# Kernel optimization log

Measured on AMD Instinct MI355X. Metric: run time of the kernel, lower is better.

The kernel has to match this reference:

```python
import jax, jax.numpy as jnp
import numpy as np

B, S, R, H = 64, 256, 196, 1024

def setup_inputs() -> dict:
    key = jax.random.key(0)
    ks = jax.random.split(key, 12)
    s = 0.02
    return {
        "dns_feature": jax.random.normal(ks[0], (B, S, H), jnp.float32),
        "img_features": jax.random.normal(ks[1], (B, R, H), jnp.float32),
        "W_dns1": jax.random.normal(ks[2], (H, H), jnp.float32) * s,
        "b_dns1": jax.random.normal(ks[3], (H,), jnp.float32) * s,
        "W_img1": jax.random.normal(ks[4], (H, H), jnp.float32) * s,
        "w_att1": jax.random.normal(ks[5], (2 * H,), jnp.float32) * s,
        "b_att1": jax.random.normal(ks[6], (), jnp.float32) * s,
        "W_dns2": jax.random.normal(ks[7], (H, H), jnp.float32) * s,
        "W_img2": jax.random.normal(ks[8], (H, H), jnp.float32) * s,
        "b_img2": jax.random.normal(ks[9], (H,), jnp.float32) * s,
        "w_att2": jax.random.normal(ks[10], (2 * H,), jnp.float32) * s,
        "b_att2": jax.random.normal(ks[11], (), jnp.float32) * s,
    }

def reference(dns_feature, img_features, W_dns1, b_dns1, W_img1, w_att1, b_att1,
              W_dns2, W_img2, b_img2, w_att2, b_att2):
    h = W_dns1.shape[0]
    # --- stage 1: textual attention (img queries over dns positions) ---
    # tanh(concat([img_proj, dns_proj])) then 2H->1 linear decomposes into
    # per-side dot products + broadcast add (repeat is position-wise redundant).
    dns_p1 = jnp.tanh(jnp.einsum('bsh,oh->bso', dns_feature, W_dns1) + b_dns1)  # (B,S,H)
    img_p1 = jnp.tanh(jnp.einsum('brh,oh->bro', img_features, W_img1))          # (B,R,H)
    s_img = img_p1 @ w_att1[:h]   # (B,R)  concat order: [img, dns]
    s_dns = dns_p1 @ w_att1[h:]   # (B,S)
    scores1 = s_img[:, :, None] + s_dns[:, None, :] + b_att1                    # (B,R,S)
    a1 = jax.nn.softmax(scores1, axis=-1)
    att_dns = jnp.einsum('brs,bsh->brh', a1, dns_feature)                       # (B,R,H)
    # --- stage 2: visual attention (attended-dns queries over img regions) ---
    dns_p2 = jnp.tanh(jnp.einsum('brh,oh->bro', att_dns, W_dns2))               # (B,R,H)
    img_p2 = jnp.tanh(jnp.einsum('brh,oh->bro', img_features, W_img2) + b_img2) # (B,R,H)
    t_dns = dns_p2 @ w_att2[:h]   # (B,R)  concat order: [dns, img]
    t_img = img_p2 @ w_att2[h:]   # (B,R)
    scores2 = t_dns[:, :, None] + t_img[:, None, :] + b_att2                    # (B,R,R)
    a2 = jax.nn.softmax(scores2, axis=-1)
    att_img = jnp.einsum('bij,bjh->bih', a2, img_features)                      # (B,R,H)
    return att_img, att_dns
```

## Files before the change

### kernel.cpp

```cpp
#include <hip/hip_runtime.h>

#define Hdim 1024
#define BB 64
#define SS 256
#define RR 196
#define MD (BB * SS)
#define MI (BB * RR)

typedef __attribute__((ext_vector_type(8))) short short8;
typedef __attribute__((ext_vector_type(4))) float floatx4;
typedef unsigned short us;

__device__ __forceinline__ unsigned short f2bf(float f) {
  unsigned int u = __float_as_uint(f);
  unsigned int r = 0x7FFFu + ((u >> 16) & 1u);
  return (unsigned short)((u + r) >> 16);
}

__device__ __forceinline__ float fast_tanh(float x) {
  x = fminf(15.f, fmaxf(-15.f, x));
  float e = __expf(2.f * x);
  return (e - 1.f) / (e + 1.f);
}

#define GLOAD16(g, l) __builtin_amdgcn_global_load_lds( \
    (const __attribute__((address_space(1))) unsigned int*)(g), \
    (__attribute__((address_space(3))) unsigned int*)(l), 16, 0, 0)

__global__ __launch_bounds__(256) void prep_kernel(
    const float4* __restrict__ dns, const float4* __restrict__ img,
    const float4* __restrict__ Wd1, const float4* __restrict__ Wi2,
    uint4* __restrict__ dns_bf, uint4* __restrict__ img_bf,
    uint4* __restrict__ wd1_bf, uint4* __restrict__ wi2_bf,
    float4* __restrict__ scz)
{
  constexpr int N0 = (MD * Hdim) / 8;
  constexpr int N1 = N0 + (MI * Hdim) / 8;
  constexpr int N2 = N1 + (Hdim * Hdim) / 8;
  constexpr int N3 = N2 + (Hdim * Hdim) / 8;
  constexpr int N4 = N3 + (MD + MI) / 8;
  const int stride = gridDim.x * 256;
  for (int i = blockIdx.x * 256 + threadIdx.x; i < N4; i += stride) {
    if (i < N3) {
      const float4* src; uint4* dst; int li;
      if (i < N0)      { src = dns; dst = dns_bf; li = i; }
      else if (i < N1) { src = img; dst = img_bf; li = i - N0; }
      else if (i < N2) { src = Wd1; dst = wd1_bf; li = i - N1; }
      else             { src = Wi2; dst = wi2_bf; li = i - N2; }
      const float4 a = src[2 * li];
      const float4 b = src[2 * li + 1];
      uint4 o;
      o.x = (unsigned)f2bf(a.x) | ((unsigned)f2bf(a.y) << 16);
      o.y = (unsigned)f2bf(a.z) | ((unsigned)f2bf(a.w) << 16);
      o.z = (unsigned)f2bf(b.x) | ((unsigned)f2bf(b.y) << 16);
      o.w = (unsigned)f2bf(b.z) | ((unsigned)f2bf(b.w) << 16);
      dst[li] = o;
    } else {
      const int li = i - N3;
      const float4 z4 = {0.f, 0.f, 0.f, 0.f};
      scz[2 * li]     = z4;
      scz[2 * li + 1] = z4;
    }
  }
}

__global__ __launch_bounds__(256) void gemm_score_bf2(
    const us* __restrict__ X1, const us* __restrict__ W1,
    const float* __restrict__ bias1, const float* __restrict__ v1, float* sc1,
    const us* __restrict__ X2, const us* __restrict__ W2,
    const float* __restrict__ bias2, const float* __restrict__ v2, float* sc2)
{
  __shared__ us Ash[2][128 * 64];
  __shared__ us Bsh[2][128 * 64];

  const int q  = gridDim.x >> 3;
  const int wg = (blockIdx.x & 7) * q + (blockIdx.x >> 3);

  const us* Xb; const us* Wb; const float* bias; const float* vatt; float* scores;
  int mt, nt;
  if (wg < (MD / 128) * 8) {
    Xb = X1; Wb = W1; bias = bias1; vatt = v1; scores = sc1;
    mt = wg >> 3; nt = wg & 7;
  } else {
    const int w2 = wg - (MD / 128) * 8;
    Xb = X2; Wb = W2; bias = bias2; vatt = v2; scores = sc2;
    mt = w2 >> 3; nt = w2 & 7;
  }
  const long m0 = (long)mt * 128;
  const long n0 = (long)nt * 128;

  const int tid  = threadIdx.x;
  const int lane = tid & 63;
  const int wave = tid >> 6;
  const int waveM = (wave >> 1) * 64;
  const int waveN = (wave & 1) * 64;

  const int rowSub  = lane >> 3;
  const int srcColE = (((lane & 7) ^ rowSub)) * 8;

  const us* gA[4]; const us* gB[4];
  int ldst[4];
  #pragma unroll
  for (int c = 0; c < 4; ++c) {
    const int r = (wave * 4 + c) * 8 + rowSub;
    gA[c] = Xb + (m0 + r) * Hdim + srcColE;
    gB[c] = Wb + (n0 + r) * Hdim + srcColE;
    ldst[c] = (wave * 4 + c) * 512 + lane * 8;
  }

  floatx4 acc[4][4];
  #pragma unroll
  for (int i = 0; i < 4; ++i)
    #pragma unroll
    for (int j = 0; j < 4; ++j)
      acc[i][j] = (floatx4){0.f, 0.f, 0.f, 0.f};

  const int frow = lane & 15;
  const int g    = lane >> 4;
  const int sw   = frow & 7;

  #pragma unroll
  for (int c = 0; c < 4; ++c) {
    GLOAD16(gA[c], &Ash[0][ldst[c]]);
    GLOAD16(gB[c], &Bsh[0][ldst[c]]);
  }
  __syncthreads();

  auto kstep = [&](int t, int pb) {
    if (t < 15) {
      const int k0 = (t + 1) * 64;
      #pragma unroll
      for (int c = 0; c < 4; ++c) {
        GLOAD16(gA[c] + k0, &Ash[pb ^ 1][ldst[c]]);
        GLOAD16(gB[c] + k0, &Bsh[pb ^ 1][ldst[c]]);
      }
    }
    #pragma unroll
    for (int ks = 0; ks < 2; ++ks) {
      const int slot = ((ks * 4 + g) ^ sw) * 8;
      short8 afr[4], bfr[4];
      #pragma unroll
      for (int mf = 0; mf < 4; ++mf)
        afr[mf] = *(const short8*)(&Ash[pb][0] + (waveM + mf * 16 + frow) * 64 + slot);
      #pragma unroll
      for (int nf = 0; nf < 4; ++nf)
        bfr[nf] = *(const short8*)(&Bsh[pb][0] + (waveN + nf * 16 + frow) * 64 + slot);
      #pragma unroll
      for (int mf = 0; mf < 4; ++mf)
        #pragma unroll
        for (int nf = 0; nf < 4; ++nf)
          acc[mf][nf] = __builtin_amdgcn_mfma_f32_16x16x32_bf16(afr[mf], bfr[nf], acc[mf][nf], 0, 0, 0);
    }
    __syncthreads();
  };

  for (int t2 = 0; t2 < 8; ++t2) {
    kstep(t2 * 2, 0);
    kstep(t2 * 2 + 1, 1);
  }

  const int rgrp = lane >> 4;
  #pragma unroll
  for (int mf = 0; mf < 4; ++mf) {
    float part[4] = {0.f, 0.f, 0.f, 0.f};
    #pragma unroll
    for (int nf = 0; nf < 4; ++nf) {
      const int n = (int)n0 + waveN + nf * 16 + (lane & 15);
      const float bi = bias[n];
      const float vv = vatt[n];
      #pragma unroll
      for (int j = 0; j < 4; ++j)
        part[j] += fast_tanh(acc[mf][nf][j] + bi) * vv;
    }
    #pragma unroll
    for (int j = 0; j < 4; ++j) {
      float s = part[j];
      s += __shfl_xor(s, 1);
      s += __shfl_xor(s, 2);
      s += __shfl_xor(s, 4);
      s += __shfl_xor(s, 8);
      if ((lane & 15) == 0) {
        const int m = (int)m0 + waveM + mf * 16 + rgrp * 4 + j;
        atomicAdd(&scores[m], s);
      }
    }
  }
}

__global__ __launch_bounds__(256) void attend_bcast(
    const float* __restrict__ sc_d, const us* __restrict__ dns_bf,
    const float* __restrict__ sc_i, const us* __restrict__ img_bf,
    float* __restrict__ out)
{
  __shared__ float p[256];
  __shared__ float red[256];
  const int b  = blockIdx.x;
  const int h0 = blockIdx.y * 512;
  const int z  = blockIdx.z;
  const int L  = z ? RR : SS;
  const float* scores = z ? sc_i : sc_d;
  const us*    feat   = z ? img_bf : dns_bf;
  float* outp = out + (z ? (size_t)0 : (size_t)BB * RR * Hdim);
  const int t = threadIdx.x;

  const float sc = (t < L) ? scores[b * L + t] : -1e30f;
  red[t] = sc;
  __syncthreads();
  for (int off = 128; off > 0; off >>= 1) {
    if (t < off) red[t] = fmaxf(red[t], red[t + off]);
    __syncthreads();
  }
  const float mx = red[0];
  __syncthreads();
  const float e = (t < L) ? __expf(sc - mx) : 0.f;
  red[t] = e;
  __syncthreads();
  for (int off = 128; off > 0; off >>= 1) {
    if (t < off) red[t] += red[t + off];
    __syncthreads();
  }
  p[t] = e / red[0];
  __syncthreads();

  const int h = h0 + 2 * t;
  const us* fb = feat + (size_t)b * L * Hdim + h;
  float a0 = 0.f, a1 = 0.f;
  #pragma unroll 8
  for (int s = 0; s < L; ++s) {
    const unsigned u = *(const unsigned*)(fb + (size_t)s * Hdim);
    const float f0 = __uint_as_float(u << 16);
    const float f1 = __uint_as_float(u & 0xffff0000u);
    a0 += p[s] * f0;
    a1 += p[s] * f1;
  }

  float* ob = outp + (size_t)b * RR * Hdim + h;
  const float2 v = make_float2(a0, a1);
  #pragma unroll 4
  for (int r = 0; r < RR; ++r)
    *(float2*)(ob + (size_t)r * Hdim) = v;
}

__global__ __launch_bounds__(256) void gemm_score(
    const float* __restrict__ X, const float* __restrict__ W,
    const float* __restrict__ bias, const float* __restrict__ vatt,
    float* __restrict__ scores)
{
  __shared__ us Ash[128 * 32];
  __shared__ us Bsh[128 * 32];
  const int tid  = threadIdx.x;
  const int lane = tid & 63;
  const int wave = tid >> 6;
  const int waveM = (wave >> 1) * 64;
  const int waveN = (wave & 1) * 64;
  const long m0 = (long)blockIdx.x * 128;
  const long n0 = (long)blockIdx.y * 128;
  const int ldRow   = tid >> 3;
  const int ldChunk = (tid & 7) * 4;

  floatx4 acc[4][4];
  #pragma unroll
  for (int i = 0; i < 4; ++i)
    #pragma unroll
    for (int j = 0; j < 4; ++j)
      acc[i][j] = (floatx4){0.f, 0.f, 0.f, 0.f};

  const int frow = lane & 15;
  const int fk   = (lane >> 4) * 8;

  for (int k0 = 0; k0 < Hdim; k0 += 32) {
    __syncthreads();
    #pragma unroll
    for (int p = 0; p < 4; ++p) {
      const int r = ldRow + p * 32;
      const float4 av = *(const float4*)&X[(m0 + r) * Hdim + k0 + ldChunk];
      const float4 bv = *(const float4*)&W[(n0 + r) * Hdim + k0 + ldChunk];
      uint2 ap, bp;
      ap.x = (unsigned)f2bf(av.x) | ((unsigned)f2bf(av.y) << 16);
      ap.y = (unsigned)f2bf(av.z) | ((unsigned)f2bf(av.w) << 16);
      bp.x = (unsigned)f2bf(bv.x) | ((unsigned)f2bf(bv.y) << 16);
      bp.y = (unsigned)f2bf(bv.z) | ((unsigned)f2bf(bv.w) << 16);
      *(uint2*)&Ash[r * 32 + ldChunk] = ap;
      *(uint2*)&Bsh[r * 32 + ldChunk] = bp;
    }
    __syncthreads();
    short8 afr[4], bfr[4];
    #pragma unroll
    for (int mf = 0; mf < 4; ++mf)
      afr[mf] = *(const short8*)&Ash[(waveM + mf * 16 + frow) * 32 + fk];
    #pragma unroll
    for (int nf = 0; nf < 4; ++nf)
      bfr[nf] = *(const short8*)&Bsh[(waveN + nf * 16 + frow) * 32 + fk];
    #pragma unroll
    for (int mf = 0; mf < 4; ++mf)
      #pragma unroll
      for (int nf = 0; nf < 4; ++nf)
        acc[mf][nf] = __builtin_amdgcn_mfma_f32_16x16x32_bf16(afr[mf], bfr[nf], acc[mf][nf], 0, 0, 0);
  }

  const int rgrp = lane >> 4;
  #pragma unroll
  for (int mf = 0; mf < 4; ++mf) {
    float part[4] = {0.f, 0.f, 0.f, 0.f};
    #pragma unroll
    for (int nf = 0; nf < 4; ++nf) {
      const int n = (int)n0 + waveN + nf * 16 + (lane & 15);
      const float bi = bias[n];
      const float vv = vatt[n];
      #pragma unroll
      for (int j = 0; j < 4; ++j)
        part[j] += fast_tanh(acc[mf][nf][j] + bi) * vv;
    }
    #pragma unroll
    for (int j = 0; j < 4; ++j) {
      float s = part[j];
      s += __shfl_xor(s, 1);
      s += __shfl_xor(s, 2);
      s += __shfl_xor(s, 4);
      s += __shfl_xor(s, 8);
      if ((lane & 15) == 0) {
        const int m = (int)m0 + waveM + mf * 16 + rgrp * 4 + j;
        atomicAdd(&scores[m], s);
      }
    }
  }
}

template <int L>
__global__ __launch_bounds__(256) void softmax_attend(
    const float* __restrict__ scores, const float* __restrict__ feat,
    float* __restrict__ attended)
{
  __shared__ float p[256];
  __shared__ float red[256];
  const int b  = blockIdx.x;
  const int h0 = blockIdx.y * 256;
  const int t  = threadIdx.x;

  const float sc = (t < L) ? scores[b * L + t] : -1e30f;
  red[t] = sc;
  __syncthreads();
  for (int off = 128; off > 0; off >>= 1) {
    if (t < off) red[t] = fmaxf(red[t], red[t + off]);
    __syncthreads();
  }
  const float mx = red[0];
  __syncthreads();
  const float e = (t < L) ? __expf(sc - mx) : 0.f;
  red[t] = e;
  __syncthreads();
  for (int off = 128; off > 0; off >>= 1) {
    if (t < off) red[t] += red[t + off];
    __syncthreads();
  }
  p[t] = e / red[0];
  __syncthreads();

  const int h = h0 + t;
  const float* fb = feat + (size_t)b * L * Hdim + h;
  float acc = 0.f;
  #pragma unroll 4
  for (int s = 0; s < L; ++s)
    acc += p[s] * fb[(size_t)s * Hdim];
  attended[b * Hdim + h] = acc;
}

__global__ __launch_bounds__(256) void broadcast_out(
    const float4* __restrict__ att_img, const float4* __restrict__ att_dns,
    float4* __restrict__ out)
{
  const int H4 = Hdim / 4;
  const long region_sz = (long)BB * RR * H4;
  const long total = 2 * region_sz;
  for (long i = (long)blockIdx.x * blockDim.x + threadIdx.x; i < total;
       i += (long)gridDim.x * blockDim.x) {
    const int region = (i >= region_sz);
    const long rem = i - (long)region * region_sz;
    const int b  = (int)(rem / (RR * H4));
    const int h4 = (int)(rem % H4);
    const float4* src = region ? att_dns : att_img;
    out[i] = src[b * H4 + h4];
  }
}

extern "C" void kernel_launch(void* const* d_in, const int* in_sizes, int n_in,
                              void* d_out, int out_size, void* d_ws, size_t ws_size,
                              hipStream_t stream) {
  const float* dns    = (const float*)d_in[0];
  const float* img    = (const float*)d_in[1];
  const float* W_dns1 = (const float*)d_in[2];
  const float* b_dns1 = (const float*)d_in[3];
  const float* w_att1 = (const float*)d_in[5];
  const float* W_img2 = (const float*)d_in[8];
  const float* b_img2 = (const float*)d_in[9];
  const float* w_att2 = (const float*)d_in[10];

  const size_t dnsB = (size_t)MD * Hdim * 2;
  const size_t imgB = (size_t)MI * Hdim * 2;
  const size_t wB   = (size_t)Hdim * Hdim * 2;
  const size_t scoresB = (16384 + 12544) * sizeof(float);
  const size_t need = dnsB + imgB + 2 * wB + scoresB;

  dim3 blk(256);

  if (ws_size >= need) {
    char* cur = (char*)d_ws;
    us* dns_bf = (us*)cur; cur += dnsB;
    us* img_bf = (us*)cur; cur += imgB;
    us* Wd1_bf = (us*)cur; cur += wB;
    us* Wi2_bf = (us*)cur; cur += wB;
    float* s_dns = (float*)cur;
    float* t_img = s_dns + 16384;

    prep_kernel<<<2048, blk, 0, stream>>>(
        (const float4*)dns, (const float4*)img,
        (const float4*)W_dns1, (const float4*)W_img2,
        (uint4*)dns_bf, (uint4*)img_bf, (uint4*)Wd1_bf, (uint4*)Wi2_bf,
        (float4*)s_dns);

    gemm_score_bf2<<<dim3((MD / 128 + MI / 128) * 8), blk, 0, stream>>>(
        dns_bf, Wd1_bf, b_dns1, w_att1 + Hdim, s_dns,
        img_bf, Wi2_bf, b_img2, w_att2 + Hdim, t_img);

    attend_bcast<<<dim3(BB, Hdim / 512, 2), blk, 0, stream>>>(
        s_dns, dns_bf, t_img, img_bf, (float*)d_out);
  } else {
    float* ws    = (float*)d_ws;
    float* s_dns = ws;
    float* t_img = ws + 16384;
    float* att_d = ws + 16384 + 12544;
    float* att_i = att_d + BB * Hdim;

    hipMemsetAsync(s_dns, 0, (16384 + 12544) * sizeof(float), stream);

    gemm_score<<<dim3(MD / 128, Hdim / 128), blk, 0, stream>>>(
        dns, W_dns1, b_dns1, w_att1 + Hdim, s_dns);
    gemm_score<<<dim3(MI / 128, Hdim / 128), blk, 0, stream>>>(
        img, W_img2, b_img2, w_att2 + Hdim, t_img);

    softmax_attend<SS><<<dim3(BB, Hdim / 256), blk, 0, stream>>>(s_dns, dns, att_d);
    softmax_attend<RR><<<dim3(BB, Hdim / 256), blk, 0, stream>>>(t_img, img, att_i);

    broadcast_out<<<2048, blk, 0, stream>>>((const float4*)att_i, (const float4*)att_d,
                                            (float4*)d_out);
  }
}
```

Before: 173.9 us.

## Restructure GEMM K-loop with explicit vmcnt waits to keep two stages in flight

Replaces the __syncthreads-based double buffer with an explicit schedule in which two K-stages are issued up front. Each compute step waits with s_waitcnt vmcnt(8) only for the older stage and uses raw s_barrier, so the next stage's global-to-LDS loads stay outstanding during the MFMAs. The goal is to stop draining all memory operations at every barrier, as __syncthreads forces. The risk is correctness if the vmcnt counts or the compiler's ordering around the empty asm memory fences do not hold.

```diff
diff --git a/kernel.cpp b/kernel.cpp
--- a/kernel.cpp
+++ b/kernel.cpp
@@ -26,6 +26,8 @@
 #define GLOAD16(g, l) __builtin_amdgcn_global_load_lds( \
     (const __attribute__((address_space(1))) unsigned int*)(g), \
     (__attribute__((address_space(3))) unsigned int*)(l), 16, 0, 0)
+
+#define MEMFENCE asm volatile("" ::: "memory")
 
 __global__ __launch_bounds__(256) void prep_kernel(
     const float4* __restrict__ dns, const float4* __restrict__ img,
@@ -119,22 +121,16 @@
   const int g    = lane >> 4;
   const int sw   = frow & 7;
 
-  #pragma unroll
-  for (int c = 0; c < 4; ++c) {
-    GLOAD16(gA[c], &Ash[0][ldst[c]]);
-    GLOAD16(gB[c], &Bsh[0][ldst[c]]);
-  }
-  __syncthreads();
-
-  auto kstep = [&](int t, int pb) {
-    if (t < 15) {
-      const int k0 = (t + 1) * 64;
-      #pragma unroll
-      for (int c = 0; c < 4; ++c) {
-        GLOAD16(gA[c] + k0, &Ash[pb ^ 1][ldst[c]]);
-        GLOAD16(gB[c] + k0, &Bsh[pb ^ 1][ldst[c]]);
-      }
-    }
+  auto stage = [&](int t, int pb) {
+    const int k0 = t * 64;
+    #pragma unroll
+    for (int c = 0; c < 4; ++c) {
+      GLOAD16(gA[c] + k0, &Ash[pb][ldst[c]]);
+      GLOAD16(gB[c] + k0, &Bsh[pb][ldst[c]]);
+    }
+  };
+
+  auto compute = [&](int pb) {
     #pragma unroll
     for (int ks = 0; ks < 2; ++ks) {
       const int slot = ((ks * 4 + g) ^ sw) * 8;
@@ -151,13 +147,41 @@
         for (int nf = 0; nf < 4; ++nf)
           acc[mf][nf] = __builtin_amdgcn_mfma_f32_16x16x32_bf16(afr[mf], bfr[nf], acc[mf][nf], 0, 0, 0);
     }
-    __syncthreads();
   };
 
-  for (int t2 = 0; t2 < 8; ++t2) {
-    kstep(t2 * 2, 0);
-    kstep(t2 * 2 + 1, 1);
-  }
+  stage(0, 0);
+  stage(1, 1);
+
+  #pragma unroll 1
+  for (int t2 = 0; t2 < 7; ++t2) {
+    asm volatile("s_waitcnt vmcnt(8)" ::: "memory");
+    __builtin_amdgcn_s_barrier();
+    MEMFENCE;
+    compute(0);
+    MEMFENCE;
+    __builtin_amdgcn_s_barrier();
+    MEMFENCE;
+    stage(2 * t2 + 2, 0);
+    asm volatile("s_waitcnt vmcnt(8)" ::: "memory");
+    __builtin_amdgcn_s_barrier();
+    MEMFENCE;
+    compute(1);
+    MEMFENCE;
+    __builtin_amdgcn_s_barrier();
+    MEMFENCE;
+    stage(2 * t2 + 3, 1);
+  }
+  asm volatile("s_waitcnt vmcnt(8)" ::: "memory");
+  __builtin_amdgcn_s_barrier();
+  MEMFENCE;
+  compute(0);
+  MEMFENCE;
+  __builtin_amdgcn_s_barrier();
+  MEMFENCE;
+  asm volatile("s_waitcnt vmcnt(0)" ::: "memory");
+  __builtin_amdgcn_s_barrier();
+  MEMFENCE;
+  compute(1);
 
   const int rgrp = lane >> 4;
   #pragma unroll
```

After: 163.2 us. 6.2% less time.
